# Optimization experiments

Measured on AMD Instinct MI355X. Metric: run time of the kernel, lower is better.

## Reference

```python
import jax, jax.numpy as jnp
import numpy as np

N = 32768      # total nodes
E = 262144     # total edges
B = 32         # graphs in batch
NP = N // B    # nodes per graph (equal-sized graphs)
K = 820        # ceil(0.8 * NP), PyG TopKPooling k
H, C = 8, 64   # heads, per-head channels
NEG_SLOPE = 0.2


def setup_inputs() -> dict:
    key = jax.random.key(0)
    ks = jax.random.split(key, 12)
    s = 0.05
    return {
        "x": jax.random.normal(ks[0], (N, 256), jnp.float32),
        "edge_attr": jax.random.normal(ks[1], (E, 32), jnp.float32),
        "Wl": jax.random.normal(ks[2], (256, H * C), jnp.float32) * s,
        "bl": jax.random.normal(ks[3], (H * C,), jnp.float32) * s,
        "Wr": jax.random.normal(ks[4], (256, H * C), jnp.float32) * s,
        "br": jax.random.normal(ks[5], (H * C,), jnp.float32) * s,
        "We": jax.random.normal(ks[6], (32, H * C), jnp.float32) * s,
        "att": jax.random.normal(ks[7], (H, C), jnp.float32) * s,
        "bias": jax.random.normal(ks[8], (H * C,), jnp.float32) * s,
        "pool_w": jax.random.normal(ks[9], (H * C,), jnp.float32),
        "edge_index": jax.random.randint(ks[10], (2, E), 0, N, jnp.int32),
    }


def reference(x, edge_attr, Wl, bl, Wr, br, We, att, bias, pool_w, edge_index):
    src, dst = edge_index[0], edge_index[1]
    # GATv2Conv (eval mode, dropout off)
    xl = (x @ Wl + bl).reshape(N, H, C)   # x_j side (lin_l)
    xr = (x @ Wr + br).reshape(N, H, C)   # x_i side (lin_r)
    e = (edge_attr @ We).reshape(E, H, C)  # lin_edge, bias=False
    m = jax.nn.leaky_relu(xl[src] + xr[dst] + e, NEG_SLOPE)   # [E,H,C]
    alpha = jnp.einsum('ehc,hc->eh', m, att)                  # [E,H]
    amax = jax.ops.segment_max(alpha, dst, num_segments=N)
    ex = jnp.exp(alpha - amax[dst])
    denom = jax.ops.segment_sum(ex, dst, num_segments=N)
    alpha = ex / denom[dst]                                   # segment softmax over dst
    out = jax.ops.segment_sum(alpha[..., None] * xl[src], dst, num_segments=N)
    h = jax.nn.relu(out.reshape(N, H * C) + bias)             # [N,512]
    # TopKPooling: score = tanh(x.w / ||w||), keep top-k per graph, scale kept rows
    score = jnp.tanh(h @ pool_w / jnp.sqrt(jnp.sum(pool_w * pool_w)))
    vals, idx = jax.lax.top_k(score.reshape(B, NP), K)        # [B,K]
    hg = h.reshape(B, NP, H * C)
    hsel = jnp.take_along_axis(hg, idx[..., None], axis=1) * vals[..., None]  # [B,K,512]
    # global max pool || global mean pool
    gmp = hsel.max(axis=1)
    gap = hsel.mean(axis=1)
    return jnp.concatenate([gmp, gap], axis=1)                # [B,1024]
```

## Files before the change

### kernel.cpp

```cpp
#include <hip/hip_runtime.h>
#include <hip/hip_bf16.h>
#include <cstdint>
#include <cstddef>

#define N_NODES 32768
#define N_EDGES 262144
#define BGRAPH  32
#define NPG     1024
#define KSEL    820
#define NEG     0.2f

typedef unsigned short u16;
typedef __attribute__((ext_vector_type(4))) float f32x4;
typedef __attribute__((ext_vector_type(8))) short s16x8;

static __device__ __forceinline__ u16 f2bf(float v) {
    __hip_bfloat16 b(v);
    return *reinterpret_cast<u16*>(&b);
}
static __device__ __forceinline__ float bf2f(u16 u) {
    __hip_bfloat16 b = *reinterpret_cast<__hip_bfloat16*>(&u);
    return (float)b;
}

typedef const __attribute__((address_space(1))) void* gas_p;
typedef __attribute__((address_space(3))) void* las_p;
static __device__ __forceinline__ void gload16(const void* g, void* l) {
    __builtin_amdgcn_global_load_lds((gas_p)g, (las_p)l, 16, 0, 0);
}

__global__ __launch_bounds__(256) void k_split_x(
    const float* __restrict__ x, u16* __restrict__ xhi, u16* __restrict__ xlo)
{
    const int i = blockIdx.x * 256 + threadIdx.x;
    const float4 v = *(const float4*)&x[(size_t)i * 4];
    u16 h0 = f2bf(v.x), h1 = f2bf(v.y), h2 = f2bf(v.z), h3 = f2bf(v.w);
    u16 l0 = f2bf(v.x - bf2f(h0));
    u16 l1 = f2bf(v.y - bf2f(h1));
    u16 l2 = f2bf(v.z - bf2f(h2));
    u16 l3 = f2bf(v.w - bf2f(h3));
    *(ushort4*)&xhi[(size_t)i * 4] = make_ushort4(h0, h1, h2, h3);
    *(ushort4*)&xlo[(size_t)i * 4] = make_ushort4(l0, l1, l2, l3);
}

__global__ __launch_bounds__(256) void k_pack_bt(
    const float* __restrict__ Wl, const float* __restrict__ Wr,
    u16* __restrict__ BpT)
{
    const int kp = blockIdx.x * 256 + threadIdx.x;
    const int n  = blockIdx.y;
    if (kp >= 768) return;
    const float* W = (n < 512) ? Wl : Wr;
    const int col = n & 511;
    const int k = kp & 255;
    const float v = W[(size_t)k * 512 + col];
    const u16 h = f2bf(v);
    const u16 o = (kp >= 256 && kp < 512) ? f2bf(v - bf2f(h)) : h;
    BpT[(size_t)n * 768 + kp] = o;
}

__global__ __launch_bounds__(256) void gemm_mfma(
    const u16* __restrict__ xhi, const u16* __restrict__ xlo,
    const u16* __restrict__ BpT,
    const float* __restrict__ bl, const float* __restrict__ br,
    float* __restrict__ xl, float* __restrict__ xr)
{
    __shared__ u16 As[128 * 64];
    __shared__ u16 Bs[128 * 64];

    const int raw = blockIdx.x;
    const int swz = (raw & 7) * 256 + (raw >> 3);
    const int mt = swz & 255, nt = swz >> 8;
    const int m0 = mt * 128, n0 = nt * 128;

    const int tid  = threadIdx.x;
    const int lane = tid & 63;
    const int wid  = tid >> 6;
    const int wr   = wid >> 1, wc = wid & 1;
    const int lr   = lane & 15;
    const int lk   = lane >> 4;

    f32x4 acc[4][4] = {};

    for (int tk = 0; tk < 12; ++tk) {
        const u16* asrc = (tk < 8) ? xhi : xlo;
        const int  kcol = (tk & 3) * 64;
        __syncthreads();
#pragma unroll
        for (int p = 0; p < 4; ++p) {
            const int c   = p * 256 + wid * 64 + lane;
            const int row = c >> 3;
            const int cs  = ((c & 7) ^ (row & 7)) * 8;
            gload16(&asrc[(size_t)(m0 + row) * 256 + kcol + cs],
                    &As[(size_t)(p * 256 + wid * 64) * 8]);
            gload16(&BpT[(size_t)(n0 + row) * 768 + tk * 64 + cs],
                    &Bs[(size_t)(p * 256 + wid * 64) * 8]);
        }
        __syncthreads();
#pragma unroll
        for (int kk = 0; kk < 2; ++kk) {
            s16x8 af[4], bfr[4];
            const int akw = kk * 32 + lk * 8;
#pragma unroll
            for (int i = 0; i < 4; ++i) {
                const int arow = wr * 64 + i * 16 + lr;
                af[i]  = *(const s16x8*)&As[arow * 64 + (akw ^ ((arow & 7) << 3))];
                const int brow = wc * 64 + i * 16 + lr;
                bfr[i] = *(const s16x8*)&Bs[brow * 64 + (akw ^ ((brow & 7) << 3))];
            }
#pragma unroll
            for (int i = 0; i < 4; ++i)
#pragma unroll
                for (int j = 0; j < 4; ++j)
                    acc[i][j] = __builtin_amdgcn_mfma_f32_16x16x32_bf16(
                        af[i], bfr[j], acc[i][j], 0, 0, 0);
        }
    }

    float* const outp = (n0 < 512) ? xl : xr;
    const int ocol0 = n0 & 511;
    const float* const bb = (n0 < 512) ? bl : br;
#pragma unroll
    for (int j = 0; j < 4; ++j) {
        const int col = ocol0 + wc * 64 + j * 16 + lr;
        const float bv = bb[col];
#pragma unroll
        for (int i = 0; i < 4; ++i) {
#pragma unroll
            for (int r = 0; r < 4; ++r) {
                const int rowg = m0 + wr * 64 + i * 16 + (lane >> 4) * 4 + r;
                outp[(size_t)rowg * 512 + col] = acc[i][j][r] + bv;
            }
        }
    }
}

__global__ void k_hist(const int* __restrict__ ei, int* __restrict__ counts)
{
    int e = blockIdx.x * 256 + threadIdx.x;
    if (e < N_EDGES) atomicAdd(&counts[ei[N_EDGES + e]], 1);
}

__global__ __launch_bounds__(1024) void k_scan(
    const int* __restrict__ counts, int* __restrict__ offsets, int* __restrict__ cursors)
{
    __shared__ int part[1024];
    const int tid = threadIdx.x;
    const int base = tid * 32;
    int loc[32];
    int s = 0;
#pragma unroll
    for (int i = 0; i < 32; ++i) { loc[i] = s; s += counts[base + i]; }
    part[tid] = s;
    __syncthreads();
    const int own = s;
    for (int off = 1; off < 1024; off <<= 1) {
        int v = (tid >= off) ? part[tid - off] : 0;
        __syncthreads();
        part[tid] += v;
        __syncthreads();
    }
    const int pre = part[tid] - own;
#pragma unroll
    for (int i = 0; i < 32; ++i) {
        int o = pre + loc[i];
        offsets[base + i] = o;
        cursors[base + i] = o;
    }
}

__global__ void k_scatter(const int* __restrict__ ei, int* __restrict__ cursors,
                          int* __restrict__ sorted_src, int* __restrict__ sorted_dst,
                          int* __restrict__ sorted_eid)
{
    int e = blockIdx.x * 256 + threadIdx.x;
    if (e >= N_EDGES) return;
    int d = ei[N_EDGES + e];
    int pos = atomicAdd(&cursors[d], 1);
    sorted_src[pos] = ei[e];
    sorted_dst[pos] = d;
    sorted_eid[pos] = e;
}

#define LT_TILES 8

__global__ __launch_bounds__(256, 4) void k_logit(
    const float* __restrict__ xl, const float* __restrict__ xr,
    const float* __restrict__ ea, const float* __restrict__ We,
    const float* __restrict__ att,
    const int* __restrict__ sorted_src, const int* __restrict__ sorted_dst,
    const int* __restrict__ sorted_eid,
    float* __restrict__ logits)
{
    __shared__ u16 Ws[128 * 104];
    __shared__ u16 Ae[64 * 104];
    __shared__ int eid_s[64], src_s[64], dst_s[64];

    const int tid  = threadIdx.x;
    const int lane = tid & 63;
    const int wid  = tid >> 6;
    const int slab = blockIdx.y;
    const int lr   = lane & 15;
    const int lk   = lane >> 4;

    for (int idx = tid; idx < 128 * 96; idx += 256) {
        const int ch = idx / 96, kp = idx % 96;
        const int k = (kp < 32) ? kp : ((kp < 64) ? kp - 32 : kp - 64);
        const float v = We[(size_t)k * 512 + slab * 128 + ch];
        const u16 h = f2bf(v);
        Ws[ch * 104 + kp] = (kp >= 64) ? f2bf(v - bf2f(h)) : h;
    }
    float attw[8];
#pragma unroll
    for (int f = 0; f < 8; ++f) attw[f] = att[slab * 128 + f * 16 + lr];

    for (int t = 0; t < LT_TILES; ++t) {
        const int ebase = (blockIdx.x * LT_TILES + t) * 64;
        __syncthreads();
        if (tid < 64) {
            eid_s[tid] = sorted_eid[ebase + tid];
            src_s[tid] = sorted_src[ebase + tid];
            dst_s[tid] = sorted_dst[ebase + tid];
        }
        __syncthreads();
        for (int idx = tid; idx < 64 * 32; idx += 256) {
            const int r = idx >> 5, k = idx & 31;
            const float v = ea[(size_t)eid_s[r] * 32 + k];
            const u16 h = f2bf(v);
            Ae[r * 104 + k]      = h;
            Ae[r * 104 + 32 + k] = f2bf(v - bf2f(h));
            Ae[r * 104 + 64 + k] = h;
        }
        __syncthreads();

        f32x4 acc[8] = {};
#pragma unroll
        for (int ks = 0; ks < 3; ++ks) {
            const s16x8 afr = *(const s16x8*)&Ae[(wid * 16 + lr) * 104 + ks * 32 + lk * 8];
#pragma unroll
            for (int f = 0; f < 8; ++f) {
                const s16x8 bfr = *(const s16x8*)&Ws[(f * 16 + lr) * 104 + ks * 32 + lk * 8];
                acc[f] = __builtin_amdgcn_mfma_f32_16x16x32_bf16(afr, bfr, acc[f], 0, 0, 0);
            }
        }

        float p0[4], p1[4];
#pragma unroll
        for (int r = 0; r < 4; ++r) { p0[r] = 0.f; p1[r] = 0.f; }
#pragma unroll
        for (int r = 0; r < 4; ++r) {
            const int el = wid * 16 + lk * 4 + r;
            const size_t sb = (size_t)src_s[el] * 512 + slab * 128 + lr;
            const size_t db = (size_t)dst_s[el] * 512 + slab * 128 + lr;
#pragma unroll
            for (int f = 0; f < 8; ++f) {
                const float z = acc[f][r] + xl[sb + f * 16] + xr[db + f * 16];
                const float tt = z > 0.f ? z : NEG * z;
                if (f < 4) p0[r] += attw[f] * tt;
                else       p1[r] += attw[f] * tt;
            }
        }
#pragma unroll
        for (int o = 1; o < 16; o <<= 1) {
#pragma unroll
            for (int r = 0; r < 4; ++r) {
                p0[r] += __shfl_xor(p0[r], o);
                p1[r] += __shfl_xor(p1[r], o);
            }
        }
        if (lr == 0) {
#pragma unroll
            for (int r = 0; r < 4; ++r) {
                const size_t eg = ebase + wid * 16 + lk * 4 + r;
                logits[eg * 8 + slab * 2]     = p0[r];
                logits[eg * 8 + slab * 2 + 1] = p1[r];
            }
        }
    }
}

#define AGG_DPB 8

__global__ __launch_bounds__(256, 8) void k_agg(
    const float* __restrict__ xl, const float* __restrict__ logits,
    const int* __restrict__ sorted_src,
    const int* __restrict__ offsets, const int* __restrict__ counts,
    const float* __restrict__ bias, const float* __restrict__ pw,
    float* __restrict__ h, float* __restrict__ score)
{
    __shared__ float red_s[4];

    const int tid = threadIdx.x;
    const int wv  = tid >> 6;
    const int l   = tid & 63;
    const int c0  = tid * 2;
    const int head = tid >> 5;

    const float2 bv  = *(const float2*)&bias[c0];
    const float2 pwv = *(const float2*)&pw[c0];

    float nrm = pwv.x * pwv.x + pwv.y * pwv.y;
#pragma unroll
    for (int o = 1; o < 64; o <<= 1) nrm += __shfl_xor(nrm, o);
    if (l == 0) red_s[wv] = nrm;
    __syncthreads();
    const float inv_nrm = 1.0f / sqrtf(red_s[0] + red_s[1] + red_s[2] + red_s[3]);

    for (int dd = 0; dd < AGG_DPB; ++dd) {
        const int d   = blockIdx.x * AGG_DPB + dd;
        const int off = offsets[d];
        const int deg = counts[d];

        float m = -INFINITY;
        for (int j = 0; j < deg; ++j)
            m = fmaxf(m, logits[(size_t)(off + j) * 8 + head]);

        float den = 0.f, a0 = 0.f, a1 = 0.f;
        for (int j = 0; j < deg; ++j) {
            const float lg = logits[(size_t)(off + j) * 8 + head];
            const int   s  = sorted_src[off + j];
            const float2 xl2 = *(const float2*)&xl[(size_t)s * 512 + c0];
            const float pe = __expf(lg - m);
            den += pe;
            a0 += pe * xl2.x;
            a1 += pe * xl2.y;
        }

        const float r = den > 0.f ? 1.0f / den : 0.f;
        const float h0 = fmaxf(a0 * r + bv.x, 0.f);
        const float h1 = fmaxf(a1 * r + bv.y, 0.f);
        *(float2*)&h[(size_t)d * 512 + c0] = make_float2(h0, h1);

        float ps = h0 * pwv.x + h1 * pwv.y;
#pragma unroll
        for (int o = 1; o < 64; o <<= 1) ps += __shfl_xor(ps, o);
        __syncthreads();
        if (l == 0) red_s[wv] = ps;
        __syncthreads();
        if (tid == 0)
            score[d] = tanhf((red_s[0] + red_s[1] + red_s[2] + red_s[3]) * inv_nrm);
    }
}

__global__ __launch_bounds__(256) void k_topk(const float* __restrict__ score,
                                              int* __restrict__ sel_idx,
                                              float* __restrict__ sel_val)
{
    __shared__ unsigned long long key[1024];
    const int g = blockIdx.x, tid = threadIdx.x;
    for (int i = tid; i < 1024; i += 256) {
        float s = score[g * 1024 + i];
        unsigned u = __float_as_uint(s);
        u = (u & 0x80000000u) ? ~u : (u | 0x80000000u);
        key[i] = ((unsigned long long)(~u) << 32) | (unsigned)i;
    }
    __syncthreads();
    for (int k = 2; k <= 1024; k <<= 1) {
        for (int j = k >> 1; j > 0; j >>= 1) {
            for (int i = tid; i < 1024; i += 256) {
                int ixj = i ^ j;
                if (ixj > i) {
                    bool up = ((i & k) == 0);
                    unsigned long long a = key[i], b = key[ixj];
                    if ((a > b) == up) { key[i] = b; key[ixj] = a; }
                }
            }
            __syncthreads();
        }
    }
    for (int kk = tid; kk < KSEL; kk += 256) {
        int idx = (int)(key[kk] & 0xFFFFFFFFu);
        sel_idx[g * KSEL + kk] = idx;
        sel_val[g * KSEL + kk] = score[g * 1024 + idx];
    }
}

#define KSLICE 103

__global__ __launch_bounds__(256) void k_pool_part(
    const float* __restrict__ h, const int* __restrict__ sel_idx,
    const float* __restrict__ sel_val, float* __restrict__ part)
{
    const int g = blockIdx.x >> 3, sl = blockIdx.x & 7;
    const int kbeg = sl * KSLICE;
    const int kend = min(KSEL, kbeg + KSLICE);
    const int n = kend - kbeg;
    __shared__ float vs[KSLICE];
    __shared__ int   is_[KSLICE];
    const int tid = threadIdx.x;
    if (tid < n) {
        vs[tid]  = sel_val[g * KSEL + kbeg + tid];
        is_[tid] = sel_idx[g * KSEL + kbeg + tid];
    }
    __syncthreads();
    const int c0 = tid, c1 = tid + 256;
    float mx0 = -INFINITY, mx1 = -INFINITY, s0 = 0.f, s1 = 0.f;
    for (int kk = 0; kk < n; ++kk) {
        const float* hp = h + ((size_t)(g * 1024 + is_[kk])) * 512;
        const float v = vs[kk];
        float f0 = hp[c0] * v, f1 = hp[c1] * v;
        mx0 = fmaxf(mx0, f0); s0 += f0;
        mx1 = fmaxf(mx1, f1); s1 += f1;
    }
    const size_t base = ((size_t)blockIdx.x * 2) * 512;
    part[base + c0] = mx0;        part[base + c1] = mx1;
    part[base + 512 + c0] = s0;   part[base + 512 + c1] = s1;
}

__global__ __launch_bounds__(256) void k_pool_merge(
    const float* __restrict__ part, float* __restrict__ out)
{
    const int g = blockIdx.x, tid = threadIdx.x;
    const int c0 = tid, c1 = tid + 256;
    float mx0 = -INFINITY, mx1 = -INFINITY, s0 = 0.f, s1 = 0.f;
    for (int sl = 0; sl < 8; ++sl) {
        const size_t base = ((size_t)(g * 8 + sl) * 2) * 512;
        mx0 = fmaxf(mx0, part[base + c0]); mx1 = fmaxf(mx1, part[base + c1]);
        s0 += part[base + 512 + c0];       s1 += part[base + 512 + c1];
    }
    out[(size_t)g * 1024 + c0] = mx0;
    out[(size_t)g * 1024 + c1] = mx1;
    out[(size_t)g * 1024 + 512 + c0] = s0 * (1.f / KSEL);
    out[(size_t)g * 1024 + 512 + c1] = s1 * (1.f / KSEL);
}

extern "C" void kernel_launch(void* const* d_in, const int* in_sizes, int n_in,
                              void* d_out, int out_size, void* d_ws, size_t ws_size,
                              hipStream_t stream)
{
    const float* x    = (const float*)d_in[0];
    const float* ea   = (const float*)d_in[1];
    const float* Wl   = (const float*)d_in[2];
    const float* bl   = (const float*)d_in[3];
    const float* Wr   = (const float*)d_in[4];
    const float* br   = (const float*)d_in[5];
    const float* We   = (const float*)d_in[6];
    const float* att  = (const float*)d_in[7];
    const float* bias = (const float*)d_in[8];
    const float* pw   = (const float*)d_in[9];
    const int*   ei   = (const int*)d_in[10];
    float* out = (float*)d_out;

    float* xl        = (float*)d_ws;
    float* xr        = xl + (size_t)N_NODES * 512;
    float* h         = xr + (size_t)N_NODES * 512;
    float* logits    = h + (size_t)N_NODES * 512;
    float* sel_val   = logits + (size_t)N_EDGES * 8;
    float* part      = sel_val + BGRAPH * KSEL;
    float* score     = part + 256 * 2 * 512;
    int* counts      = (int*)(score + N_NODES);
    int* offsets     = counts + N_NODES;
    int* cursors     = offsets + N_NODES;
    int* sorted_src  = cursors + N_NODES;
    int* sorted_dst  = sorted_src + N_EDGES;
    int* sorted_eid  = sorted_dst + N_EDGES;
    int* sel_idx     = sorted_eid + N_EDGES;
    u16* xhi         = (u16*)(sel_idx + BGRAPH * KSEL);
    u16* xlo         = xhi + (size_t)N_NODES * 256;
    u16* bpt         = xlo + (size_t)N_NODES * 256;

    hipMemsetAsync(counts, 0, (size_t)N_NODES * sizeof(int), stream);

    k_split_x<<<(N_NODES * 256) / (4 * 256), 256, 0, stream>>>(x, xhi, xlo);
    k_pack_bt<<<dim3(3, 1024), 256, 0, stream>>>(Wl, Wr, bpt);
    gemm_mfma<<<2048, 256, 0, stream>>>(xhi, xlo, bpt, bl, br, xl, xr);

    k_hist<<<N_EDGES / 256, 256, 0, stream>>>(ei, counts);
    k_scan<<<1, 1024, 0, stream>>>(counts, offsets, cursors);
    k_scatter<<<N_EDGES / 256, 256, 0, stream>>>(ei, cursors, sorted_src, sorted_dst, sorted_eid);
    k_logit<<<dim3(N_EDGES / 64 / LT_TILES, 4), 256, 0, stream>>>(
        xl, xr, ea, We, att, sorted_src, sorted_dst, sorted_eid, logits);
    k_agg<<<N_NODES / AGG_DPB, 256, 0, stream>>>(xl, logits, sorted_src, offsets, counts,
                                                 bias, pw, h, score);
    k_topk<<<BGRAPH, 256, 0, stream>>>(score, sel_idx, sel_val);
    k_pool_part<<<BGRAPH * 8, 256, 0, stream>>>(h, sel_idx, sel_val, part);
    k_pool_merge<<<BGRAPH, 256, 0, stream>>>(part, out);
}
```

Measured before the change: 605.3 us.

## Restructure split-bf16 GEMM and pre-pack edge features to single bf16

The node GEMM now loads hi and lo parts of A and B in a single k-pass and issues three MFMAs (hh, hl, lh) per tile, instead of concatenating them along K over 12 tiles. This removes the redundant repeated load of xhi and shrinks the packed weight matrix. The edge-logit kernel drops the hi/lo split for edge_attr and We and uses plain bf16, pre-packed in swizzled layout by two new prep kernels, so the logit kernel does one MFMA k-step and loads tiles asynchronously. This lowers logit precision and adds an extra pass that writes a gathered bf16 copy of edge_attr.

```diff
diff --git a/kernel.cpp b/kernel.cpp
--- a/kernel.cpp
+++ b/kernel.cpp
@@ -49,14 +49,24 @@
 {
     const int kp = blockIdx.x * 256 + threadIdx.x;
     const int n  = blockIdx.y;
-    if (kp >= 768) return;
     const float* W = (n < 512) ? Wl : Wr;
     const int col = n & 511;
     const int k = kp & 255;
     const float v = W[(size_t)k * 512 + col];
     const u16 h = f2bf(v);
-    const u16 o = (kp >= 256 && kp < 512) ? f2bf(v - bf2f(h)) : h;
-    BpT[(size_t)n * 768 + kp] = o;
+    const u16 o = (kp >= 256) ? f2bf(v - bf2f(h)) : h;
+    BpT[(size_t)n * 512 + kp] = o;
+}
+
+__global__ __launch_bounds__(256) void k_prep_we(
+    const float* __restrict__ We, u16* __restrict__ webf)
+{
+    const int g = blockIdx.x * 256 + threadIdx.x;
+    const int slab = g >> 12, ch = (g >> 5) & 127, kk = g & 31;
+    const int c = kk >> 3, j = kk & 7;
+    const int s = (ch & 3) ^ ((ch >> 2) & 3);
+    const int ksrc = ((c ^ s) << 3) + j;
+    webf[g] = f2bf(We[(size_t)ksrc * 512 + slab * 128 + ch]);
 }
 
 __global__ __launch_bounds__(256) void gemm_mfma(
@@ -65,8 +75,10 @@
     const float* __restrict__ bl, const float* __restrict__ br,
     float* __restrict__ xl, float* __restrict__ xr)
 {
-    __shared__ u16 As[128 * 64];
-    __shared__ u16 Bs[128 * 64];
+    __shared__ u16 Ahs[128 * 32];
+    __shared__ u16 Als[128 * 32];
+    __shared__ u16 Bhs[128 * 32];
+    __shared__ u16 Bls[128 * 32];
 
     const int raw = blockIdx.x;
     const int swz = (raw & 7) * 256 + (raw >> 3);
@@ -82,39 +94,41 @@
 
     f32x4 acc[4][4] = {};
 
-    for (int tk = 0; tk < 12; ++tk) {
-        const u16* asrc = (tk < 8) ? xhi : xlo;
-        const int  kcol = (tk & 3) * 64;
-        __syncthreads();
-#pragma unroll
-        for (int p = 0; p < 4; ++p) {
-            const int c   = p * 256 + wid * 64 + lane;
-            const int row = c >> 3;
-            const int cs  = ((c & 7) ^ (row & 7)) * 8;
-            gload16(&asrc[(size_t)(m0 + row) * 256 + kcol + cs],
-                    &As[(size_t)(p * 256 + wid * 64) * 8]);
-            gload16(&BpT[(size_t)(n0 + row) * 768 + tk * 64 + cs],
-                    &Bs[(size_t)(p * 256 + wid * 64) * 8]);
-        }
-        __syncthreads();
-#pragma unroll
-        for (int kk = 0; kk < 2; ++kk) {
-            s16x8 af[4], bfr[4];
-            const int akw = kk * 32 + lk * 8;
-#pragma unroll
-            for (int i = 0; i < 4; ++i) {
-                const int arow = wr * 64 + i * 16 + lr;
-                af[i]  = *(const s16x8*)&As[arow * 64 + (akw ^ ((arow & 7) << 3))];
-                const int brow = wc * 64 + i * 16 + lr;
-                bfr[i] = *(const s16x8*)&Bs[brow * 64 + (akw ^ ((brow & 7) << 3))];
-            }
-#pragma unroll
-            for (int i = 0; i < 4; ++i)
-#pragma unroll
-                for (int j = 0; j < 4; ++j)
-                    acc[i][j] = __builtin_amdgcn_mfma_f32_16x16x32_bf16(
-                        af[i], bfr[j], acc[i][j], 0, 0, 0);
-        }
+    for (int q = 0; q < 8; ++q) {
+        __syncthreads();
+#pragma unroll
+        for (int half = 0; half < 2; ++half) {
+            const int w   = half * 256 + tid;
+            const int row = w >> 2, cc = w & 3;
+            const int cs  = cc ^ (row & 3) ^ ((row >> 2) & 3);
+            const int ko  = q * 32 + cs * 8;
+            gload16(&xhi[(size_t)(m0 + row) * 256 + ko],       &Ahs[w * 8]);
+            gload16(&xlo[(size_t)(m0 + row) * 256 + ko],       &Als[w * 8]);
+            gload16(&BpT[(size_t)(n0 + row) * 512 + ko],       &Bhs[w * 8]);
+            gload16(&BpT[(size_t)(n0 + row) * 512 + 256 + ko], &Bls[w * 8]);
+        }
+        __syncthreads();
+
+        s16x8 ah[4], al[4], bh[4], bl_[4];
+#pragma unroll
+        for (int i = 0; i < 4; ++i) {
+            const int ar  = wr * 64 + i * 16 + lr;
+            const int aof = ar * 32 + ((lk ^ (ar & 3) ^ ((ar >> 2) & 3)) << 3);
+            ah[i] = *(const s16x8*)&Ahs[aof];
+            al[i] = *(const s16x8*)&Als[aof];
+            const int brw = wc * 64 + i * 16 + lr;
+            const int bof = brw * 32 + ((lk ^ (brw & 3) ^ ((brw >> 2) & 3)) << 3);
+            bh[i]  = *(const s16x8*)&Bhs[bof];
+            bl_[i] = *(const s16x8*)&Bls[bof];
+        }
+#pragma unroll
+        for (int i = 0; i < 4; ++i)
+#pragma unroll
+            for (int j = 0; j < 4; ++j) {
+                acc[i][j] = __builtin_amdgcn_mfma_f32_16x16x32_bf16(ah[i], bh[j],  acc[i][j], 0, 0, 0);
+                acc[i][j] = __builtin_amdgcn_mfma_f32_16x16x32_bf16(ah[i], bl_[j], acc[i][j], 0, 0, 0);
+                acc[i][j] = __builtin_amdgcn_mfma_f32_16x16x32_bf16(al[i], bh[j],  acc[i][j], 0, 0, 0);
+            }
     }
 
     float* const outp = (n0 < 512) ? xl : xr;
@@ -128,7 +142,7 @@
         for (int i = 0; i < 4; ++i) {
 #pragma unroll
             for (int r = 0; r < 4; ++r) {
-                const int rowg = m0 + wr * 64 + i * 16 + (lane >> 4) * 4 + r;
+                const int rowg = m0 + wr * 64 + i * 16 + lk * 4 + r;
                 outp[(size_t)rowg * 512 + col] = acc[i][j][r] + bv;
             }
         }
@@ -182,19 +196,30 @@
     sorted_eid[pos] = e;
 }
 
+__global__ __launch_bounds__(256) void k_prep_ea(
+    const float* __restrict__ ea, const int* __restrict__ sorted_eid,
+    u16* __restrict__ eabf)
+{
+    const int g = blockIdx.x * 256 + threadIdx.x;
+    const int pos = g >> 5, kk = g & 31;
+    const int c = kk >> 3, j = kk & 7;
+    const int s = (pos & 3) ^ ((pos >> 2) & 3);
+    const int ksrc = ((c ^ s) << 3) + j;
+    eabf[g] = f2bf(ea[(size_t)sorted_eid[pos] * 32 + ksrc]);
+}
+
 #define LT_TILES 8
 
-__global__ __launch_bounds__(256, 4) void k_logit(
+__global__ __launch_bounds__(256, 6) void k_logit(
     const float* __restrict__ xl, const float* __restrict__ xr,
-    const float* __restrict__ ea, const float* __restrict__ We,
+    const u16* __restrict__ eabf, const u16* __restrict__ webf,
     const float* __restrict__ att,
     const int* __restrict__ sorted_src, const int* __restrict__ sorted_dst,
-    const int* __restrict__ sorted_eid,
     float* __restrict__ logits)
 {
-    __shared__ u16 Ws[128 * 104];
-    __shared__ u16 Ae[64 * 104];
-    __shared__ int eid_s[64], src_s[64], dst_s[64];
+    __shared__ u16 Ws[128 * 32];
+    __shared__ u16 Ae[64 * 32];
+    __shared__ int src_s[64], dst_s[64];
 
     const int tid  = threadIdx.x;
     const int lane = tid & 63;
@@ -203,45 +228,35 @@
     const int lr   = lane & 15;
     const int lk   = lane >> 4;
 
-    for (int idx = tid; idx < 128 * 96; idx += 256) {
-        const int ch = idx / 96, kp = idx % 96;
-        const int k = (kp < 32) ? kp : ((kp < 64) ? kp - 32 : kp - 64);
-        const float v = We[(size_t)k * 512 + slab * 128 + ch];
-        const u16 h = f2bf(v);
-        Ws[ch * 104 + kp] = (kp >= 64) ? f2bf(v - bf2f(h)) : h;
+#pragma unroll
+    for (int p = 0; p < 2; ++p) {
+        const int chunk = p * 256 + tid;
+        gload16(&webf[(size_t)slab * 4096 + chunk * 8], &Ws[chunk * 8]);
     }
     float attw[8];
 #pragma unroll
     for (int f = 0; f < 8; ++f) attw[f] = att[slab * 128 + f * 16 + lr];
+
+    const int sxor = (lr & 3) ^ (lr >> 2);
+    const int swoff = (lk ^ sxor) << 3;
 
     for (int t = 0; t < LT_TILES; ++t) {
         const int ebase = (blockIdx.x * LT_TILES + t) * 64;
         __syncthreads();
         if (tid < 64) {
-            eid_s[tid] = sorted_eid[ebase + tid];
             src_s[tid] = sorted_src[ebase + tid];
             dst_s[tid] = sorted_dst[ebase + tid];
         }
-        __syncthreads();
-        for (int idx = tid; idx < 64 * 32; idx += 256) {
-            const int r = idx >> 5, k = idx & 31;
-            const float v = ea[(size_t)eid_s[r] * 32 + k];
-            const u16 h = f2bf(v);
-            Ae[r * 104 + k]      = h;
-            Ae[r * 104 + 32 + k] = f2bf(v - bf2f(h));
-            Ae[r * 104 + 64 + k] = h;
-        }
-        __syncthreads();
-
-        f32x4 acc[8] = {};
-#pragma unroll
-        for (int ks = 0; ks < 3; ++ks) {
-            const s16x8 afr = *(const s16x8*)&Ae[(wid * 16 + lr) * 104 + ks * 32 + lk * 8];
-#pragma unroll
-            for (int f = 0; f < 8; ++f) {
-                const s16x8 bfr = *(const s16x8*)&Ws[(f * 16 + lr) * 104 + ks * 32 + lk * 8];
-                acc[f] = __builtin_amdgcn_mfma_f32_16x16x32_bf16(afr, bfr, acc[f], 0, 0, 0);
-            }
+        gload16(&eabf[(size_t)ebase * 32 + tid * 8], &Ae[tid * 8]);
+        __syncthreads();
+
+        const s16x8 afr = *(const s16x8*)&Ae[(wid * 16 + lr) * 32 + swoff];
+        f32x4 acc[8];
+#pragma unroll
+        for (int f = 0; f < 8; ++f) {
+            const s16x8 bfr = *(const s16x8*)&Ws[(f * 16 + lr) * 32 + swoff];
+            acc[f] = __builtin_amdgcn_mfma_f32_16x16x32_bf16(
+                afr, bfr, (f32x4){0.f, 0.f, 0.f, 0.f}, 0, 0, 0);
         }
 
         float p0[4], p1[4];
@@ -458,18 +473,22 @@
     u16* xhi         = (u16*)(sel_idx + BGRAPH * KSEL);
     u16* xlo         = xhi + (size_t)N_NODES * 256;
     u16* bpt         = xlo + (size_t)N_NODES * 256;
+    u16* webf        = bpt + (size_t)1024 * 512;
+    u16* eabf        = webf + 4 * 128 * 32;
 
     hipMemsetAsync(counts, 0, (size_t)N_NODES * sizeof(int), stream);
 
     k_split_x<<<(N_NODES * 256) / (4 * 256), 256, 0, stream>>>(x, xhi, xlo);
-    k_pack_bt<<<dim3(3, 1024), 256, 0, stream>>>(Wl, Wr, bpt);
+    k_pack_bt<<<dim3(2, 1024), 256, 0, stream>>>(Wl, Wr, bpt);
+    k_prep_we<<<64, 256, 0, stream>>>(We, webf);
     gemm_mfma<<<2048, 256, 0, stream>>>(xhi, xlo, bpt, bl, br, xl, xr);
 
     k_hist<<<N_EDGES / 256, 256, 0, stream>>>(ei, counts);
     k_scan<<<1, 1024, 0, stream>>>(counts, offsets, cursors);
     k_scatter<<<N_EDGES / 256, 256, 0, stream>>>(ei, cursors, sorted_src, sorted_dst, sorted_eid);
+    k_prep_ea<<<(N_EDGES * 32) / 256, 256, 0, stream>>>(ea, sorted_eid, eabf);
     k_logit<<<dim3(N_EDGES / 64 / LT_TILES, 4), 256, 0, stream>>>(
-        xl, xr, ea, We, att, sorted_src, sorted_dst, sorted_eid, logits);
+        xl, xr, eabf, webf, att, sorted_src, sorted_dst, logits);
     k_agg<<<N_NODES / AGG_DPB, 256, 0, stream>>>(xl, logits, sorted_src, offsets, counts,
                                                  bias, pw, h, score);
     k_topk<<<BGRAPH, 256, 0, stream>>>(score, sel_idx, sel_val);
```

New measurement: 589.9 us. -2.5%, faster.
